# Performance work log

Hardware: AMD Instinct MI355X
Metric: run time of the kernel (lower is better)

Reference implementation:

```python
import jax, jax.numpy as jnp
import numpy as np

TREE_DEPTH = 6
IN_F, OUT_F = 1024, 1024
BATCH = 2048
N_LEAVES = 2 ** TREE_DEPTH
N_NODES = N_LEAVES - 1


def _tree_routes(depth):
    """Static routing table: for each leaf, the decision-node index visited at
    each depth and whether the leaf takes the sigmoid (1) or 1-sigmoid (0) branch.
    Mirrors the torch traversal: node = 2*node + 1 + bit; bits of leaf id LSB-first."""
    n_leaves = 2 ** depth
    idx = np.zeros((n_leaves, depth), dtype=np.int32)
    pos = np.zeros((n_leaves, depth), dtype=bool)
    for l in range(n_leaves):
        node, index = 0, l
        for d in range(depth):
            idx[l, d] = node
            pos[l, d] = (index % 2 == 0)
            node = node * 2 + 1 + index % 2
            index >>= 1
    return idx, pos

ROUTE_IDX, ROUTE_POS = _tree_routes(TREE_DEPTH)


def setup_inputs() -> dict:
    key = jax.random.key(0)
    kx, kwd, kwl = jax.random.split(key, 3)
    scale = 0.02  # keep sigmoid/softmax logits in a sane range
    x = jax.random.normal(kx, (BATCH, IN_F), dtype=jnp.float32)
    Wd = jax.random.normal(kwd, (N_NODES, IN_F), dtype=jnp.float32) * scale
    bd = jnp.zeros((N_NODES,), dtype=jnp.float32)
    Wl = jax.random.normal(kwl, (N_LEAVES, OUT_F, IN_F), dtype=jnp.float32) * scale
    bl = jnp.zeros((N_LEAVES, OUT_F), dtype=jnp.float32)
    return {"x": x, "Wd": Wd, "bd": bd, "Wl": Wl, "bl": bl}


def reference(x, Wd, bd, Wl, bl):
    # All decision node probabilities in one GEMM: [B, n_nodes]
    dprob = jax.nn.sigmoid(x @ Wd.T + bd)
    # Gather per-leaf path probs [B, L, depth] and take path product -> routing [B, L]
    path = dprob[:, ROUTE_IDX]                      # [B, L, D]
    path = jnp.where(ROUTE_POS, path, 1.0 - path)
    routing = jnp.prod(path, axis=-1)               # [B, L]
    # All leaf experts in one batched GEMM: [B, L, out], softmax over out (torch dim=1)
    leaf_logits = jnp.einsum('bi,loi->blo', x, Wl) + bl
    leaves = jax.nn.softmax(leaf_logits, axis=-1)
    # Routing-weighted sum over leaves
    return jnp.einsum('bl,blo->bo', routing, leaves)
```

## Files before the change

kernel.cpp:

```cpp
#include <hip/hip_runtime.h>
#include <hip/hip_bf16.h>

#define BATCH 2048
#define KD 1024
#define ND 1024
#define NLEAF 64
#define BM 256
#define BN 256

typedef __attribute__((ext_vector_type(8))) short bf16x8;
typedef __attribute__((ext_vector_type(4))) float f32x4;
typedef __attribute__((ext_vector_type(8))) _Float16 f16x8;

#define WLB_OFF 0ULL
#define XB_OFF  134217728ULL
#define RT_OFF  138412032ULL
#define LG_OFF  138936320ULL

__device__ __forceinline__ unsigned short f2bf(float f) {
  unsigned int u = __float_as_uint(f);
  u += 0x7fffu + ((u >> 16) & 1u);
  return (unsigned short)(u >> 16);
}

__device__ __forceinline__ void gload_lds16(const void* g, void* l) {
  __builtin_amdgcn_global_load_lds(
      (const __attribute__((address_space(1))) unsigned int*)g,
      (__attribute__((address_space(3))) unsigned int*)l, 16, 0, 0);
}

__global__ void __launch_bounds__(256) convert_kernel(
    const float* __restrict__ Wl, const float* __restrict__ x,
    unsigned short* __restrict__ wlb, unsigned short* __restrict__ xb) {
  const long long WL4 = 16777216LL;
  const long long X4  = 524288LL;
  long long i = (long long)blockIdx.x * 256 + threadIdx.x;
  const long long stride = (long long)gridDim.x * 256;
  for (; i < WL4 + X4; i += stride) {
    float4 v;
    if (i < WL4) v = ((const float4*)Wl)[i];
    else         v = ((const float4*)x)[i - WL4];
    ushort4 o;
    o.x = f2bf(v.x); o.y = f2bf(v.y); o.z = f2bf(v.z); o.w = f2bf(v.w);
    if (i < WL4) ((ushort4*)wlb)[i] = o;
    else         ((ushort4*)xb)[i - WL4] = o;
  }
}

__global__ void __launch_bounds__(256) routing_kernel(
    const float* __restrict__ x, const float* __restrict__ Wd,
    const float* __restrict__ bd, float* __restrict__ rt) {
  __shared__ float xs[4][KD];
  __shared__ float sdp[4][64];
  const int tid = threadIdx.x;
  const int b0 = blockIdx.x * 4;
  const float4* xsrc = (const float4*)(x + (size_t)b0 * KD);
  float4* xdst = (float4*)&xs[0][0];
  for (int i = tid; i < KD; i += 256) xdst[i] = xsrc[i];
  __syncthreads();
  const int wv = tid >> 6, ln = tid & 63;
  const int b = b0 + wv;
  if (ln < 63) {
    const float4* wrow = (const float4*)(Wd + (size_t)ln * KD);
    const float4* xr = (const float4*)&xs[wv][0];
    float4 a = {0.f, 0.f, 0.f, 0.f};
    for (int k = 0; k < KD / 4; ++k) {
      float4 w = wrow[k], xv = xr[k];
      a.x += w.x * xv.x; a.y += w.y * xv.y; a.z += w.z * xv.z; a.w += w.w * xv.w;
    }
    float z = a.x + a.y + a.z + a.w + bd[ln];
    sdp[wv][ln] = 1.f / (1.f + __expf(-z));
  }
  __syncthreads();
  float prod = 1.f;
  int node = 0, index = ln;
  for (int d = 0; d < 6; ++d) {
    float pv = sdp[wv][node];
    prod *= (index & 1) ? (1.f - pv) : pv;
    node = node * 2 + 1 + (index & 1);
    index >>= 1;
  }
  rt[(size_t)b * NLEAF + ln] = prod;
}

#define BARR  asm volatile("s_barrier" ::: "memory")
#define LGKM0 asm volatile("s_waitcnt lgkmcnt(0)" ::: "memory")
#define VMC2  asm volatile("s_waitcnt vmcnt(2)" ::: "memory")
#define VMC0  asm volatile("s_waitcnt vmcnt(0)" ::: "memory")
#define SB0   __builtin_amdgcn_sched_barrier(0)
#define PRIO1 __builtin_amdgcn_s_setprio(1)
#define PRIO0 __builtin_amdgcn_s_setprio(0)

#define RD_A(BUF, OFS)                                                       \
  _Pragma("unroll") for (int mi = 0; mi < 4; ++mi) {                         \
    aQ[mi][0] = *(const bf16x8*)((BUF) + offA[(OFS) + mi]);                  \
    aQ[mi][1] = *(const bf16x8*)((BUF) + (offA[(OFS) + mi] ^ 64));           \
  }
#define RD_B(DST, BUF, OFS)                                                  \
  _Pragma("unroll") for (int nj = 0; nj < 2; ++nj) {                         \
    DST[nj][0] = *(const bf16x8*)((BUF) + offB[(OFS) + nj]);                 \
    DST[nj][1] = *(const bf16x8*)((BUF) + (offB[(OFS) + nj] ^ 64));          \
  }
#define MFMA_Q(H, J, BR)                                                     \
  PRIO1;                                                                     \
  _Pragma("unroll") for (int mi = 0; mi < 4; ++mi)                           \
  _Pragma("unroll") for (int nj = 0; nj < 2; ++nj) {                         \
    acc[4*(H)+mi][2*(J)+nj] = __builtin_amdgcn_mfma_f32_16x16x32_bf16(       \
        aQ[mi][0], BR[nj][0], acc[4*(H)+mi][2*(J)+nj], 0, 0, 0);             \
    acc[4*(H)+mi][2*(J)+nj] = __builtin_amdgcn_mfma_f32_16x16x32_bf16(       \
        aQ[mi][1], BR[nj][1], acc[4*(H)+mi][2*(J)+nj], 0, 0, 0);             \
  }                                                                          \
  PRIO0; SB0

__global__ void __launch_bounds__(512, 2) gemm_kernel(
    const unsigned short* __restrict__ A, const unsigned short* __restrict__ B,
    const float* __restrict__ blg, _Float16* __restrict__ C, int ntile) {
  extern __shared__ char smem[];
  const int tid = threadIdx.x;
  const int w = tid >> 6, ln = tid & 63;
  const int wm = w >> 2, wn = w & 3;
  const int g = ln >> 4, r16 = ln & 15;
  const int bid = blockIdx.x;
  const int j = bid >> 3;
  const int bm = (j & 7) * BM;
  const int bn = (((j >> 3) << 3) + (bid & 7)) * BN;
  const long long ldc = (long long)ntile * 256;

  const int sr = tid >> 3, sj = tid & 7;
  const int sjx = sj ^ (sr & 7);
  const unsigned short* gA = A + (size_t)(bm + sr) * KD + (size_t)sjx * 8;
  const unsigned short* gB = B + (size_t)(bn + sr) * KD + (size_t)sjx * 8;
  const int ldsw = w * 1024;

  auto STAGE_H = [&](int t, int which) {
    char* dst = smem + ((t & 1) << 16) + which * 16384 + ldsw;
    const unsigned short* s = ((which < 2) ? gA : gB) +
        (((size_t)(which & 1)) << 7) * KD + ((size_t)t << 6);
    gload_lds16(s, dst);
    gload_lds16(s + (size_t)64 * KD, dst + 8192);
  };

  const int swz = (g ^ (r16 & 7)) * 16;
  int offA[8], offB[4];
#pragma unroll
  for (int mi = 0; mi < 8; ++mi)
    offA[mi] = wm * 16384 + (mi * 16 + r16) * 128 + swz;
#pragma unroll
  for (int ni = 0; ni < 4; ++ni)
    offB[ni] = (2 + (wn >> 1)) * 16384 + ((wn & 1) * 64 + ni * 16 + r16) * 128 + swz;

  f32x4 acc[8][4];
#pragma unroll
  for (int mi = 0; mi < 8; ++mi)
#pragma unroll
    for (int ni = 0; ni < 4; ++ni) acc[mi][ni] = (f32x4){0.f, 0.f, 0.f, 0.f};

  const char* b0 = smem;
  const char* b1 = smem + 65536;
  bf16x8 aQ[4][2], b01[2][2], b23[2][2];

  STAGE_H(0, 0); STAGE_H(0, 1); STAGE_H(0, 2); STAGE_H(0, 3);
  STAGE_H(1, 0);
  VMC2; BARR;

  for (int i = 0; i < 8; ++i) {
    const int t0 = 2 * i, t1 = 2 * i + 1;
    const bool pf = (i < 7);
    RD_A(b0, 0); RD_B(b01, b0, 0);
    STAGE_H(t1, 1);
    BARR; LGKM0; SB0;
    MFMA_Q(0, 0, b01);
    BARR;
    RD_B(b23, b0, 2);
    STAGE_H(t1, 2);
    BARR; LGKM0; SB0;
    MFMA_Q(0, 1, b23);
    BARR;
    RD_A(b0, 4);
    STAGE_H(t1, 3);
    BARR; LGKM0; SB0;
    MFMA_Q(1, 0, b01);
    BARR;
    if (pf) { STAGE_H(t0 + 2, 0); VMC2; } else { VMC0; }
    BARR;
    MFMA_Q(1, 1, b23);
    BARR;
    RD_A(b1, 0); RD_B(b01, b1, 0);
    if (pf) STAGE_H(t0 + 2, 1);
    BARR; LGKM0; SB0;
    MFMA_Q(0, 0, b01);
    BARR;
    RD_B(b23, b1, 2);
    if (pf) STAGE_H(t0 + 2, 2);
    BARR; LGKM0; SB0;
    MFMA_Q(0, 1, b23);
    BARR;
    RD_A(b1, 4);
    if (pf) STAGE_H(t0 + 2, 3);
    BARR; LGKM0; SB0;
    MFMA_Q(1, 0, b01);
    BARR;
    if (pf) STAGE_H(t0 + 3, 0);
    VMC2;
    BARR;
    MFMA_Q(1, 1, b23);
    if (pf) BARR;
  }

  const int lf = bn >> 10;
  float blv[4];
#pragma unroll
  for (int ni = 0; ni < 4; ++ni)
    blv[ni] = blg[(size_t)lf * ND + (bn & 1023) + wn * 64 + ni * 16 + r16];
#pragma unroll
  for (int mi = 0; mi < 8; ++mi)
#pragma unroll
    for (int q = 0; q < 4; ++q) {
      const long long grow = bm + wm * 128 + mi * 16 + g * 4 + q;
#pragma unroll
      for (int ni = 0; ni < 4; ++ni) {
        const int gcol = bn + wn * 64 + ni * 16 + r16;
        C[grow * ldc + gcol] = (_Float16)(acc[mi][ni][q] + blv[ni]);
      }
    }
}

__global__ void __launch_bounds__(256) smax_kernel(
    const _Float16* __restrict__ Cg, const float* __restrict__ rt,
    float* __restrict__ out, int lpg, int l0, int first) {
  const int tid = threadIdx.x;
  const int wv = tid >> 6, ln = tid & 63;
  const int b = blockIdx.x * 4 + wv;
  const long long ldc = (long long)lpg * ND;
  const _Float16* base = Cg + (size_t)b * ldc + ln * 8;
  const float rtv = (ln < lpg) ? rt[(size_t)b * NLEAF + l0 + ln] : 0.f;

  float oacc[16];
#pragma unroll
  for (int k = 0; k < 16; ++k) oacc[k] = 0.f;

  for (int jj = 0; jj < lpg; ++jj) {
    const f16x8 h0 = *(const f16x8*)(base + jj * ND);
    const f16x8 h1 = *(const f16x8*)(base + jj * ND + 512);
    float e[16], s = 0.f;
#pragma unroll
    for (int k = 0; k < 8; ++k) { e[k] = __expf((float)h0[k]); s += e[k]; }
#pragma unroll
    for (int k = 0; k < 8; ++k) { e[8 + k] = __expf((float)h1[k]); s += e[8 + k]; }
#pragma unroll
    for (int off = 1; off < 64; off <<= 1) s += __shfl_xor(s, off);
    const float coef = __shfl(rtv, jj) / s;
#pragma unroll
    for (int k = 0; k < 16; ++k) oacc[k] += coef * e[k];
  }

  float* o0 = out + (size_t)b * ND + ln * 8;
  if (first) {
    *(float4*)o0         = (float4){oacc[0], oacc[1], oacc[2], oacc[3]};
    *(float4*)(o0 + 4)   = (float4){oacc[4], oacc[5], oacc[6], oacc[7]};
    *(float4*)(o0 + 512) = (float4){oacc[8], oacc[9], oacc[10], oacc[11]};
    *(float4*)(o0 + 516) = (float4){oacc[12], oacc[13], oacc[14], oacc[15]};
  } else {
#pragma unroll
    for (int part = 0; part < 4; ++part) {
      float* p = o0 + (part >> 1) * 512 + (part & 1) * 4;
      float4 v = *(const float4*)p;
      v.x += oacc[part * 4 + 0]; v.y += oacc[part * 4 + 1];
      v.z += oacc[part * 4 + 2]; v.w += oacc[part * 4 + 3];
      *(float4*)p = v;
    }
  }
}

extern "C" void kernel_launch(void* const* d_in, const int* in_sizes, int n_in,
                              void* d_out, int out_size, void* d_ws, size_t ws_size,
                              hipStream_t stream) {
  const float* x  = (const float*)d_in[0];
  const float* Wd = (const float*)d_in[1];
  const float* bd = (const float*)d_in[2];
  const float* Wl = (const float*)d_in[3];
  const float* bl = (const float*)d_in[4];
  float* out = (float*)d_out;
  char* ws = (char*)d_ws;
  unsigned short* wlb = (unsigned short*)(ws + WLB_OFF);
  unsigned short* xb  = (unsigned short*)(ws + XB_OFF);
  float* rt           = (float*)(ws + RT_OFF);
  _Float16* lg        = (_Float16*)(ws + LG_OFF);

  convert_kernel<<<2048, 256, 0, stream>>>(Wl, x, wlb, xb);
  routing_kernel<<<BATCH / 4, 256, 0, stream>>>(x, Wd, bd, rt);
  hipFuncSetAttribute((const void*)gemm_kernel,
                      hipFuncAttributeMaxDynamicSharedMemorySize, 131072);

  const int ngrp = (ws_size >= LG_OFF + (size_t)BATCH * NLEAF * ND * 2) ? 1 : 4;
  const int lpg = NLEAF / ngrp;
  const int ntile = lpg * (ND / BN);
  for (int grp = 0; grp < ngrp; ++grp) {
    gemm_kernel<<<8 * ntile, 512, 131072, stream>>>(
        xb, wlb + (size_t)grp * lpg * ND * KD,
        bl + (size_t)grp * lpg * ND, lg, ntile);
    smax_kernel<<<BATCH / 4, 256, 0, stream>>>(lg, rt, out,
                                               lpg, grp * lpg, grp == 0);
  }
}
```

Baseline: 524.4 us.

## Deepen GEMM prefetch pipeline and fix leaf grouping to two passes

The GEMM main loop now issues global-to-LDS staging further ahead, keeping up to four outstanding loads (vmcnt 4 instead of 2) and reordering which half-tiles are staged during each MFMA quarter. This is meant to hide more global memory latency behind the MFMA work. Separately, the launch now always splits the 64 leaves into two groups of 32 instead of choosing 1 or 4 groups from the workspace size. That changes the intermediate logits buffer footprint and the number of smax launches, and assumes the workspace holds half the leaf logits.

Measured after the change: 467.0 us. 1.12x faster.

```diff
diff --git a/kernel.cpp b/kernel.cpp
--- a/kernel.cpp
+++ b/kernel.cpp
@@ -5,6 +5,8 @@
 #define KD 1024
 #define ND 1024
 #define NLEAF 64
+#define NGRP 2
+#define LPG 32
 #define BM 256
 #define BN 256
 
@@ -85,7 +87,7 @@
 
 #define BARR  asm volatile("s_barrier" ::: "memory")
 #define LGKM0 asm volatile("s_waitcnt lgkmcnt(0)" ::: "memory")
-#define VMC2  asm volatile("s_waitcnt vmcnt(2)" ::: "memory")
+#define VMC4  asm volatile("s_waitcnt vmcnt(4)" ::: "memory")
 #define VMC0  asm volatile("s_waitcnt vmcnt(0)" ::: "memory")
 #define SB0   __builtin_amdgcn_sched_barrier(0)
 #define PRIO1 __builtin_amdgcn_s_setprio(1)
@@ -160,48 +162,47 @@
   bf16x8 aQ[4][2], b01[2][2], b23[2][2];
 
   STAGE_H(0, 0); STAGE_H(0, 1); STAGE_H(0, 2); STAGE_H(0, 3);
-  STAGE_H(1, 0);
-  VMC2; BARR;
+  STAGE_H(1, 2); STAGE_H(1, 3);
+  VMC4; BARR;
 
   for (int i = 0; i < 8; ++i) {
-    const int t0 = 2 * i, t1 = 2 * i + 1;
+    const int t1 = 2 * i + 1, t2 = 2 * i + 2, t3 = 2 * i + 3;
     const bool pf = (i < 7);
     RD_A(b0, 0); RD_B(b01, b0, 0);
+    STAGE_H(t1, 0);
+    BARR; LGKM0; SB0;
+    MFMA_Q(0, 0, b01);
+    BARR;
+    RD_B(b23, b0, 2);
     STAGE_H(t1, 1);
     BARR; LGKM0; SB0;
+    MFMA_Q(0, 1, b23);
+    BARR;
+    RD_A(b0, 4);
+    if (pf) STAGE_H(t2, 2);
+    BARR; LGKM0; SB0;
+    MFMA_Q(1, 0, b01);
+    BARR;
+    if (pf) { STAGE_H(t2, 3); VMC4; } else { VMC0; }
+    BARR;
+    MFMA_Q(1, 1, b23);
+    BARR;
+    RD_A(b1, 0); RD_B(b01, b1, 0);
+    if (pf) STAGE_H(t2, 0);
+    BARR; LGKM0; SB0;
     MFMA_Q(0, 0, b01);
     BARR;
-    RD_B(b23, b0, 2);
-    STAGE_H(t1, 2);
+    RD_B(b23, b1, 2);
+    if (pf) STAGE_H(t2, 1);
     BARR; LGKM0; SB0;
     MFMA_Q(0, 1, b23);
     BARR;
-    RD_A(b0, 4);
-    STAGE_H(t1, 3);
+    RD_A(b1, 4);
+    if (pf) STAGE_H(t3, 2);
     BARR; LGKM0; SB0;
     MFMA_Q(1, 0, b01);
     BARR;
-    if (pf) { STAGE_H(t0 + 2, 0); VMC2; } else { VMC0; }
-    BARR;
-    MFMA_Q(1, 1, b23);
-    BARR;
-    RD_A(b1, 0); RD_B(b01, b1, 0);
-    if (pf) STAGE_H(t0 + 2, 1);
-    BARR; LGKM0; SB0;
-    MFMA_Q(0, 0, b01);
-    BARR;
-    RD_B(b23, b1, 2);
-    if (pf) STAGE_H(t0 + 2, 2);
-    BARR; LGKM0; SB0;
-    MFMA_Q(0, 1, b23);
-    BARR;
-    RD_A(b1, 4);
-    if (pf) STAGE_H(t0 + 2, 3);
-    BARR; LGKM0; SB0;
-    MFMA_Q(1, 0, b01);
-    BARR;
-    if (pf) STAGE_H(t0 + 3, 0);
-    VMC2;
+    if (pf) { STAGE_H(t3, 3); VMC4; }
     BARR;
     MFMA_Q(1, 1, b23);
     if (pf) BARR;
@@ -292,14 +293,12 @@
   hipFuncSetAttribute((const void*)gemm_kernel,
                       hipFuncAttributeMaxDynamicSharedMemorySize, 131072);
 
-  const int ngrp = (ws_size >= LG_OFF + (size_t)BATCH * NLEAF * ND * 2) ? 1 : 4;
-  const int lpg = NLEAF / ngrp;
-  const int ntile = lpg * (ND / BN);
-  for (int grp = 0; grp < ngrp; ++grp) {
+  const int ntile = LPG * (ND / BN);
+  for (int grp = 0; grp < NGRP; ++grp) {
     gemm_kernel<<<8 * ntile, 512, 131072, stream>>>(
-        xb, wlb + (size_t)grp * lpg * ND * KD,
-        bl + (size_t)grp * lpg * ND, lg, ntile);
+        xb, wlb + (size_t)grp * LPG * ND * KD,
+        bl + (size_t)grp * LPG * ND, lg, ntile);
     smax_kernel<<<BATCH / 4, 256, 0, stream>>>(lg, rt, out,
-                                               lpg, grp * lpg, grp == 0);
-  }
-}
+                                               LPG, grp * LPG, grp == 0);
+  }
+}
```
